# Kernel optimization log

Measured on AMD Instinct MI355X. Metric: run time of the kernel, lower is better.

The kernel has to match this reference:

```python
import jax, jax.numpy as jnp
import numpy as np

N = 100000
E = 1600000
F_IN = 128
HDIM = 64
HEADS = 8
C1 = HDIM // HEADS  # 8 per-head channels in conv1
NUM_CLASSES = 2
NUM_GRAPHS = 64
NEG_SLOPE = 0.2


def setup_inputs() -> dict:
    key = jax.random.key(0)
    ks = jax.random.split(key, 12)
    x = jax.random.normal(ks[0], (N, F_IN), dtype=jnp.float32)
    edge_index = jax.random.randint(ks[1], (2, E), 0, N, dtype=jnp.int64)
    batch = jnp.sort(jax.random.randint(ks[2], (N,), 0, NUM_GRAPHS, dtype=jnp.int64))
    # conv1 params (Glorot-ish scale)
    W1 = jax.random.normal(ks[3], (F_IN, HEADS * C1), dtype=jnp.float32) * (1.0 / np.sqrt(F_IN))
    att_src1 = jax.random.normal(ks[4], (HEADS, C1), dtype=jnp.float32) * 0.1
    att_dst1 = jax.random.normal(ks[5], (HEADS, C1), dtype=jnp.float32) * 0.1
    b1 = jnp.zeros((HEADS * C1,), dtype=jnp.float32)
    # conv2 params (1 head, no concat)
    W2 = jax.random.normal(ks[6], (HDIM, 1 * NUM_CLASSES), dtype=jnp.float32) * (1.0 / np.sqrt(HDIM))
    att_src2 = jax.random.normal(ks[7], (1, NUM_CLASSES), dtype=jnp.float32) * 0.1
    att_dst2 = jax.random.normal(ks[8], (1, NUM_CLASSES), dtype=jnp.float32) * 0.1
    b2 = jnp.zeros((NUM_CLASSES,), dtype=jnp.float32)
    return {"x": x, "edge_index": edge_index, "batch": batch,
            "W1": W1, "att_src1": att_src1, "att_dst1": att_dst1, "b1": b1,
            "W2": W2, "att_src2": att_src2, "att_dst2": att_dst2, "b2": b2}


def gat_conv(x, src, dst, W, a_src, a_dst, b, heads, ch, concat):
    # PyG GATConv: linear proj -> per-edge attention -> segment softmax over dst -> scatter-add
    n = x.shape[0]
    h = (x @ W).reshape(n, heads, ch)                      # [N,H,C]
    alpha_s = jnp.einsum('nhc,hc->nh', h, a_src)           # [N,H]
    alpha_d = jnp.einsum('nhc,hc->nh', h, a_dst)           # [N,H]
    e = jax.nn.leaky_relu(alpha_s[src] + alpha_d[dst], NEG_SLOPE)  # [E,H]
    m = jax.ops.segment_max(e, dst, num_segments=n)        # stable softmax per dst
    e = jnp.exp(e - m[dst])
    denom = jax.ops.segment_sum(e, dst, num_segments=n) + 1e-16
    alpha = e / denom[dst]                                 # [E,H]
    msg = h[src] * alpha[:, :, None]                       # [E,H,C]
    out = jax.ops.segment_sum(msg, dst, num_segments=n)    # [N,H,C]
    if concat:
        out = out.reshape(n, heads * ch)
    else:
        out = out.mean(axis=1)
    return out + b


def reference(x, edge_index, batch, W1, att_src1, att_dst1, b1, W2, att_src2, att_dst2, b2):
    # PyG GATConv default add_self_loops=True
    loops = jnp.arange(N, dtype=edge_index.dtype)
    src = jnp.concatenate([edge_index[0], loops])
    dst = jnp.concatenate([edge_index[1], loops])
    h = gat_conv(x, src, dst, W1, att_src1, att_dst1, b1, HEADS, C1, concat=True)
    h = jax.nn.relu(h)
    # F.dropout with training=False (eval mode) -> identity
    h = gat_conv(h, src, dst, W2, att_src2, att_dst2, b2, 1, NUM_CLASSES, concat=False)
    # global_mean_pool over batch ids
    sums = jax.ops.segment_sum(h, batch, num_segments=NUM_GRAPHS)
    cnts = jax.ops.segment_sum(jnp.ones((N,), h.dtype), batch, num_segments=NUM_GRAPHS)
    pooled = sums / jnp.maximum(cnts, 1.0)[:, None]        # [G, num_classes]
    return jax.nn.log_softmax(pooled, axis=1)
```

## Files before the change

### kernel.cpp

```cpp
#include <hip/hip_runtime.h>
#include <hip/hip_bf16.h>
#include <hip/hip_fp16.h>
#include <math.h>

#define NN 100000
#define EE 1600000
#define ET 1700000
#define NEG_SLOPE 0.2f
#define XS_STRIDE 136
#define L2E 1.44269504088896f

#define BKB 8
#define BKSZ 256
#define NBUCK 391
#define SLAB 8192
#define PAD 32
#define EPT2 16
#define CHUNK2 (256 * EPT2)
#define NCH2 ((ET + CHUNK2 - 1) / CHUNK2)

typedef _Float16 f16;
typedef f16 f16x8 __attribute__((ext_vector_type(8)));
typedef float f32x4 __attribute__((ext_vector_type(4)));
typedef float f32x2 __attribute__((ext_vector_type(2)));

__device__ __forceinline__ float leaky(float v) {
    return v > 0.f ? v : NEG_SLOPE * v;
}
__device__ __forceinline__ unsigned char enc_fp8(float v) {
    int pk = __builtin_amdgcn_cvt_pk_fp8_f32(v, 0.f, 0, false);
    return (unsigned char)(pk & 0xff);
}


__global__ __launch_bounds__(256) void convert_w_kernel(
        const float* __restrict__ W1, f16* __restrict__ wt,
        unsigned char* __restrict__ nrec) {
    int i = blockIdx.x * 256 + threadIdx.x;
    if (i < 128 * 64) {
        int n = i >> 7, k = i & 127;
        wt[n * 128 + k] = (f16)W1[k * 64 + n];
    }
    if (blockIdx.x == 0 && threadIdx.x < 8) {
        uint4* dr = (uint4*)(nrec + (size_t)NN * 128);
        dr[threadIdx.x] = make_uint4(0u, 0u, 0xFC00u, 0u);
    }
}

__global__ __launch_bounds__(256) void gemm1_mfma(
        const float* __restrict__ x, const f16* __restrict__ wt,
        const float* __restrict__ att_s, const float* __restrict__ att_d,
        unsigned char* __restrict__ nrec) {
    __shared__ f16 xs[64 * XS_STRIDE];
    const int tid = threadIdx.x;
    const int node0 = blockIdx.x * 64;
    for (int i = tid; i < 64 * 64; i += 256) {
        int r = i >> 6, cp = i & 63;
        int n = node0 + r;
        float2 v = (n < NN) ? ((const float2*)x)[(long)n * 64 + cp]
                            : make_float2(0.f, 0.f);
        xs[r * XS_STRIDE + 2 * cp]     = (f16)v.x;
        xs[r * XS_STRIDE + 2 * cp + 1] = (f16)v.y;
    }
    __syncthreads();
    const int wv = tid >> 6;
    const int lane = tid & 63;
    const int n16 = lane & 15;
    const int quad = lane >> 4;
    f16x8 bf[4][4];
#pragma unroll
    for (int t = 0; t < 4; ++t)
#pragma unroll
        for (int kk = 0; kk < 4; ++kk)
            bf[t][kk] = *(const f16x8*)(wt + ((t * 16 + n16) * 128 + kk * 32 + quad * 8));
    f32x4 acc[4] = {{0,0,0,0},{0,0,0,0},{0,0,0,0},{0,0,0,0}};
#pragma unroll
    for (int kk = 0; kk < 4; ++kk) {
        f16x8 af = *(const f16x8*)(xs + ((wv * 16 + n16) * XS_STRIDE + kk * 32 + quad * 8));
#pragma unroll
        for (int t = 0; t < 4; ++t)
            acc[t] = __builtin_amdgcn_mfma_f32_16x16x32_f16(af, bf[t][kk], acc[t], 0, 0, 0);
    }
    float ats[4], atd[4];
#pragma unroll
    for (int t = 0; t < 4; ++t) {
        ats[t] = att_s[t * 16 + n16];
        atd[t] = att_d[t * 16 + n16];
    }
    const int head = (n16 >> 3);
    const int chpos = n16 & 7;
#pragma unroll
    for (int t = 0; t < 4; ++t)
#pragma unroll
        for (int r = 0; r < 4; ++r) {
            int m = node0 + wv * 16 + quad * 4 + r;
            bool ok = (m < NN);
            if (ok)
                nrec[(size_t)m * 128 + (t * 2 + head) * 16 + chpos] =
                    enc_fp8(acc[t][r]);
            float vs = acc[t][r] * ats[t];
            float vd = acc[t][r] * atd[t];
            vs += __shfl_xor(vs, 1, 64); vd += __shfl_xor(vd, 1, 64);
            vs += __shfl_xor(vs, 2, 64); vd += __shfl_xor(vd, 2, 64);
            vs += __shfl_xor(vs, 4, 64); vd += __shfl_xor(vd, 4, 64);
            if (ok && chpos == 0) {
                unsigned char* nb = nrec + (size_t)m * 128 + (t * 2 + head) * 16;
                *(__half*)(nb + 8)  = __float2half_rn(vs * L2E);
                *(float*)(nb + 12) = vd * L2E;
            }
        }
}

__global__ __launch_bounds__(256) void bucket_fill(
        const int* __restrict__ ei, int* __restrict__ bcur,
        unsigned* __restrict__ gpay) {
    __shared__ int lcnt[NBUCK];
    __shared__ int gbase[NBUCK];
    const int tid = threadIdx.x;
    for (int i = tid; i < NBUCK; i += 256) lcnt[i] = 0;
    __syncthreads();
    const int base = blockIdx.x * CHUNK2 + tid;
    unsigned pay[EPT2];
    int bk[EPT2], pos[EPT2];
#pragma unroll
    for (int k = 0; k < EPT2; ++k) {
        int e = base + k * 256;
        if (e < ET) {
            int s, d;
            if (e < EE) {
                s = __builtin_nontemporal_load(ei + e);
                d = __builtin_nontemporal_load(ei + EE + e);
            } else { s = d = e - EE; }
            int b = d >> BKB;
            bk[k] = b;
            pay[k] = ((unsigned)(d & (BKSZ - 1)) << 17) | (unsigned)s;
            pos[k] = atomicAdd(&lcnt[b], 1);
        } else bk[k] = -1;
    }
    __syncthreads();
    for (int i = tid; i < NBUCK; i += 256)
        gbase[i] = lcnt[i] ? (i * SLAB + atomicAdd(&bcur[i * PAD], lcnt[i])) : 0;
    __syncthreads();
#pragma unroll
    for (int k = 0; k < EPT2; ++k)
        if (bk[k] >= 0) gpay[gbase[bk[k]] + pos[k]] = pay[k];
}

__global__ __launch_bounds__(256) void fine_csr(
        const unsigned* __restrict__ gpay, const int* __restrict__ bcur,
        int* __restrict__ rowptr, int* __restrict__ rowend,
        int* __restrict__ csr_src) {
    __shared__ int cnt[BKSZ];
    __shared__ int ts[256];
    const int b = blockIdx.x;
    const int tid = threadIdx.x;
    const int off = b * SLAB;
    int blen = bcur[b * PAD];
    if (blen > SLAB) blen = SLAB;
    const int d0 = b << BKB;
    cnt[tid] = 0;
    __syncthreads();
    for (int i = tid; i < blen; i += 256)
        atomicAdd(&cnt[gpay[off + i] >> 17], 1);
    __syncthreads();
    int v = cnt[tid];
    int vp = (v + 7) & ~7;
    ts[tid] = vp;
    __syncthreads();
    for (int o = 1; o < 256; o <<= 1) {
        int u = (tid >= o) ? ts[tid - o] : 0;
        __syncthreads();
        ts[tid] += u;
        __syncthreads();
    }
    int excl = ts[tid] - vp;
    if (excl + vp > SLAB) vp = v;
    cnt[tid] = excl;
    int d = d0 + tid;
    if (d < NN) {
        rowptr[d] = off + excl;
        rowend[d] = off + excl + v;
    }
    for (int i = v; i < vp; ++i) csr_src[off + excl + i] = NN;
    __syncthreads();
    for (int i = tid; i < blen; i += 256) {
        unsigned pay = gpay[off + i];
        int pos = atomicAdd(&cnt[pay >> 17], 1);
        csr_src[off + pos] = (int)(pay & 0x1FFFFu);
    }
}

__global__ __launch_bounds__(256) void conv1_fused_kernel(
        const int* __restrict__ rowptr, const int* __restrict__ rowend,
        const int* __restrict__ csr_src, const unsigned char* __restrict__ nrec,
        const float* __restrict__ b1, const float* __restrict__ W2,
        const float* __restrict__ as2, const float* __restrict__ ad2,
        float4* __restrict__ rec) {
    const int tid = threadIdx.x;
    const int wv = tid >> 6;
    const int c = tid & 63;
    const int slot = c >> 3;
    const int hd = c & 7;
    int n0 = __builtin_amdgcn_readfirstlane((blockIdx.x * 4 + wv) * 2);
    int n1 = n0 + 1;
    const float adA = *(const float*)(nrec + ((size_t)n0 << 7) + (hd << 4) + 12);
    const float adB = *(const float*)(nrec + ((size_t)n1 << 7) + (hd << 4) + 12);
    int jA = rowptr[n0];
    int jB = rowptr[n1];
    int eA = jA + ((rowend[n0] - jA + 7) & ~7);
    int eB = jB + ((rowend[n1] - jB + 7) & ~7);
    float accA[8] = {0.f,0.f,0.f,0.f,0.f,0.f,0.f,0.f};
    float accB[8] = {0.f,0.f,0.f,0.f,0.f,0.f,0.f,0.f};
    float lA = 0.f, lB = 0.f;

#define STEP1(j, ad, l, acc)                                                 \
    {                                                                        \
        int src = csr_src[(j) + slot];                                       \
        uint4 v = *(const uint4*)(nrec + (((size_t)src << 7) | (hd << 4)));  \
        unsigned short ush = (unsigned short)v.z;                            \
        float as = __half2float(*(const __half*)&ush);                       \
        float p = exp2f(leaky(as + (ad)));                                   \
        f32x2 f01 = __builtin_amdgcn_cvt_pk_f32_fp8((int)v.x, 0);            \
        f32x2 f23 = __builtin_amdgcn_cvt_pk_f32_fp8((int)v.x, 1);            \
        f32x2 f45 = __builtin_amdgcn_cvt_pk_f32_fp8((int)v.y, 0);            \
        f32x2 f67 = __builtin_amdgcn_cvt_pk_f32_fp8((int)v.y, 1);            \
        (l) += p;                                                            \
        acc[0] += p * f01.x; acc[1] += p * f01.y;                            \
        acc[2] += p * f23.x; acc[3] += p * f23.y;                            \
        acc[4] += p * f45.x; acc[5] += p * f45.y;                            \
        acc[6] += p * f67.x; acc[7] += p * f67.y;                            \
        (j) += 8;                                                            \
    }

    while (jA < eA && jB < eB) {
        STEP1(jA, adA, lA, accA);
        STEP1(jB, adB, lB, accB);
    }
    while (jA < eA) STEP1(jA, adA, lA, accA);
    while (jB < eB) STEP1(jB, adB, lB, accB);
#undef STEP1

    const int sb0 = slot & 1, sb1 = slot & 2, sb2 = slot & 4;
    float h4A[4], h4B[4];
#pragma unroll
    for (int i = 0; i < 4; ++i) {
        float xa0 = accA[i]     + __shfl_xor(accA[i], 8, 64);
        float xa1 = accA[i + 4] + __shfl_xor(accA[i + 4], 8, 64);
        h4A[i] = sb0 ? xa1 : xa0;
        float xb0 = accB[i]     + __shfl_xor(accB[i], 8, 64);
        float xb1 = accB[i + 4] + __shfl_xor(accB[i + 4], 8, 64);
        h4B[i] = sb0 ? xb1 : xb0;
    }
    float h2A[2], h2B[2];
#pragma unroll
    for (int i = 0; i < 2; ++i) {
        float xa0 = h4A[i]     + __shfl_xor(h4A[i], 16, 64);
        float xa1 = h4A[i + 2] + __shfl_xor(h4A[i + 2], 16, 64);
        h2A[i] = sb1 ? xa1 : xa0;
        float xb0 = h4B[i]     + __shfl_xor(h4B[i], 16, 64);
        float xb1 = h4B[i + 2] + __shfl_xor(h4B[i + 2], 16, 64);
        h2B[i] = sb1 ? xb1 : xb0;
    }
    float ya0 = h2A[0] + __shfl_xor(h2A[0], 32, 64);
    float ya1 = h2A[1] + __shfl_xor(h2A[1], 32, 64);
    float aA = sb2 ? ya1 : ya0;
    float yb0 = h2B[0] + __shfl_xor(h2B[0], 32, 64);
    float yb1 = h2B[1] + __shfl_xor(h2B[1], 32, 64);
    float aB = sb2 ? yb1 : yb0;
    lA += __shfl_xor(lA, 8, 64); lA += __shfl_xor(lA, 16, 64); lA += __shfl_xor(lA, 32, 64);
    lB += __shfl_xor(lB, 8, 64); lB += __shfl_xor(lB, 16, 64); lB += __shfl_xor(lB, 32, 64);
    int ch = (hd << 3) + ((slot & 1) << 2) + (slot & 2) + ((slot >> 2) & 1);
    float invA = 1.f / (lA + 1e-16f);
    float invB = 1.f / (lB + 1e-16f);
    float bb = b1[ch];
    float2 w = ((const float2*)W2)[ch];
    float vA = fmaxf(aA * invA + bb, 0.f);
    float vB = fmaxf(aB * invB + bb, 0.f);
    float rA0 = vA * w.x, rA1 = vA * w.y;
    float rB0 = vB * w.x, rB1 = vB * w.y;
#pragma unroll
    for (int off = 1; off < 64; off <<= 1) {
        rA0 += __shfl_xor(rA0, off, 64);
        rA1 += __shfl_xor(rA1, off, 64);
        rB0 += __shfl_xor(rB0, off, 64);
        rB1 += __shfl_xor(rB1, off, 64);
    }
    if (c == 0) {
        rec[n0] = make_float4((rA0 * as2[0] + rA1 * as2[1]) * L2E, rA0, rA1,
                              (rA0 * ad2[0] + rA1 * ad2[1]) * L2E);
        rec[n1] = make_float4((rB0 * as2[0] + rB1 * as2[1]) * L2E, rB0, rB1,
                              (rB0 * ad2[0] + rB1 * ad2[1]) * L2E);
    }
}

__global__ __launch_bounds__(256) void conv2_pool_kernel(
        const int* __restrict__ rowptr, const int* __restrict__ rowend,
        const int* __restrict__ csr_src, const float4* __restrict__ rec,
        const int* __restrict__ batch,
        float* __restrict__ pooled ) {
    __shared__ float ls[192];
    int tid = threadIdx.x;
    if (tid < 192) ls[tid] = 0.f;
    __syncthreads();
    int n = blockIdx.x * 256 + tid;
    if (n < NN) {
        float adn = rec[n].w;
        int jb = rowptr[n], je = rowend[n];
        float l0 = 0.f, l1 = 0.f, l2 = 0.f, l3 = 0.f;
        float x0 = 0.f, x1 = 0.f, x2 = 0.f, x3 = 0.f;
        float y0 = 0.f, y1 = 0.f, y2 = 0.f, y3 = 0.f;
        int j = jb;
        for (; j + 3 < je; j += 4) {
            float4 ra = rec[csr_src[j]];
            float4 rb = rec[csr_src[j + 1]];
            float4 rc = rec[csr_src[j + 2]];
            float4 rd = rec[csr_src[j + 3]];
            float pa = exp2f(leaky(ra.x + adn));
            float pb = exp2f(leaky(rb.x + adn));
            float pc = exp2f(leaky(rc.x + adn));
            float pd = exp2f(leaky(rd.x + adn));
            l0 += pa; x0 += pa * ra.y; y0 += pa * ra.z;
            l1 += pb; x1 += pb * rb.y; y1 += pb * rb.z;
            l2 += pc; x2 += pc * rc.y; y2 += pc * rc.z;
            l3 += pd; x3 += pd * rd.y; y3 += pd * rd.z;
        }
        for (; j < je; ++j) {
            float4 ra = rec[csr_src[j]];
            float pa = exp2f(leaky(ra.x + adn));
            l0 += pa; x0 += pa * ra.y; y0 += pa * ra.z;
        }
        float l = (l0 + l1) + (l2 + l3);
        float xx = (x0 + x1) + (x2 + x3);
        float yy = (y0 + y1) + (y2 + y3);
        float inv = 1.f / (l + 1e-16f);
        int g = batch[n];
        atomicAdd(&ls[g * 2],     xx * inv);
        atomicAdd(&ls[g * 2 + 1], yy * inv);
        atomicAdd(&ls[128 + g],   1.f);
    }
    __syncthreads();
    if (tid < 192) atomicAdd(&pooled[tid], ls[tid]);
}

__global__ __launch_bounds__(64) void final_kernel(
        const float* __restrict__ pooled, const float* __restrict__ b2,
        float* __restrict__ out) {
    int g = threadIdx.x;
    if (g >= 64) return;
    float c = pooled[128 + g];
    float denom = c > 1.f ? c : 1.f;
    float p0 = pooled[g * 2] / denom + b2[0];
    float p1 = pooled[g * 2 + 1] / denom + b2[1];
    float m = fmaxf(p0, p1);
    float lse = m + logf(expf(p0 - m) + expf(p1 - m));
    out[g * 2] = p0 - lse;
    out[g * 2 + 1] = p1 - lse;
}

extern "C" void kernel_launch(void* const* d_in, const int* in_sizes, int n_in,
                              void* d_out, int out_size, void* d_ws, size_t ws_size,
                              hipStream_t stream) {
    const float* x   = (const float*)d_in[0];
    const int*   ei  = (const int*)d_in[1];
    const int*   bat = (const int*)d_in[2];
    const float* W1  = (const float*)d_in[3];
    const float* as1 = (const float*)d_in[4];
    const float* ad1 = (const float*)d_in[5];
    const float* b1  = (const float*)d_in[6];
    const float* W2  = (const float*)d_in[7];
    const float* as2 = (const float*)d_in[8];
    const float* ad2 = (const float*)d_in[9];
    const float* b2  = (const float*)d_in[10];
    float* out = (float*)d_out;

    float* ws = (float*)d_ws;
    const long off_nrec   = 0;
    const long off_wt     = off_nrec + (long)(NN + 1) * 32;
    const long off_rec    = off_wt + 4096;
    const long off_rowptr = off_rec + (long)NN * 4;
    const long off_rowend = off_rowptr + NN;
    const long off_gpay   = off_rowend + NN;
    const long off_csr    = off_gpay + (long)NBUCK * SLAB;
    const long off_zero   = off_csr + (long)NBUCK * SLAB;
    const long off_bcur   = off_zero;
    const long off_pool   = off_bcur + NBUCK * PAD;
    const long zero_elems = off_pool + 192 - off_zero;

    hipMemsetAsync(ws + off_zero, 0, zero_elems * sizeof(float), stream);

    convert_w_kernel<<<32, 256, 0, stream>>>(W1, (f16*)(ws + off_wt),
                                             (unsigned char*)(ws + off_nrec));
    gemm1_mfma<<<(NN + 63) / 64, 256, 0, stream>>>(
        x, (const f16*)(ws + off_wt), as1, ad1,
        (unsigned char*)(ws + off_nrec));

    bucket_fill<<<NCH2, 256, 0, stream>>>(ei, (int*)(ws + off_bcur),
                                          (unsigned*)(ws + off_gpay));
    fine_csr<<<NBUCK, 256, 0, stream>>>(
        (const unsigned*)(ws + off_gpay), (const int*)(ws + off_bcur),
        (int*)(ws + off_rowptr), (int*)(ws + off_rowend),
        (int*)(ws + off_csr));

    conv1_fused_kernel<<<NN / 8, 256, 0, stream>>>(
        (const int*)(ws + off_rowptr), (const int*)(ws + off_rowend),
        (const int*)(ws + off_csr), (const unsigned char*)(ws + off_nrec),
        b1, W2, as2, ad2, (float4*)(ws + off_rec));

    conv2_pool_kernel<<<(NN + 255) / 256, 256, 0, stream>>>(
        (const int*)(ws + off_rowptr), (const int*)(ws + off_rowend),
        (const int*)(ws + off_csr), (const float4*)(ws + off_rec),
        bat, ws + off_pool);

    final_kernel<<<1, 64, 0, stream>>>(ws + off_pool, b2, out);
}
```

Baseline: 233.9 us.

## Process four nodes per wave in conv1 with butterfly-fold reductions and prefetch conv2 indices

```diff
diff --git a/kernel.cpp b/kernel.cpp
--- a/kernel.cpp
+++ b/kernel.cpp
@@ -25,11 +25,21 @@
 typedef float f32x2 __attribute__((ext_vector_type(2)));
 
 __device__ __forceinline__ float leaky(float v) {
-    return v > 0.f ? v : NEG_SLOPE * v;
+    return fmaxf(v, NEG_SLOPE * v);
 }
 __device__ __forceinline__ unsigned char enc_fp8(float v) {
     int pk = __builtin_amdgcn_cvt_pk_fp8_f32(v, 0.f, 0, false);
     return (unsigned char)(pk & 0xff);
+}
+
+__device__ __forceinline__ void fold8(float (&dst)[8], const float (&X)[8],
+                                      const float (&Y)[8], int sb, int off) {
+#pragma unroll
+    for (int i = 0; i < 8; ++i) {
+        float m = sb ? Y[i] : X[i];
+        float o = sb ? X[i] : Y[i];
+        dst[i] = m + __shfl_xor(o, off, 64);
+    }
 }
 
 
@@ -201,25 +211,29 @@
     const int c = tid & 63;
     const int slot = c >> 3;
     const int hd = c & 7;
-    int n0 = __builtin_amdgcn_readfirstlane((blockIdx.x * 4 + wv) * 2);
-    int n1 = n0 + 1;
-    const float adA = *(const float*)(nrec + ((size_t)n0 << 7) + (hd << 4) + 12);
-    const float adB = *(const float*)(nrec + ((size_t)n1 << 7) + (hd << 4) + 12);
-    int jA = rowptr[n0];
-    int jB = rowptr[n1];
-    int eA = jA + ((rowend[n0] - jA + 7) & ~7);
-    int eB = jB + ((rowend[n1] - jB + 7) & ~7);
-    float accA[8] = {0.f,0.f,0.f,0.f,0.f,0.f,0.f,0.f};
-    float accB[8] = {0.f,0.f,0.f,0.f,0.f,0.f,0.f,0.f};
-    float lA = 0.f, lB = 0.f;
-
-#define STEP1(j, ad, l, acc)                                                 \
+    const int sb0 = slot & 1, sb1 = (slot >> 1) & 1, sb2 = (slot >> 2) & 1;
+    int n0 = __builtin_amdgcn_readfirstlane((blockIdx.x * 4 + wv) * 4);
+    const float adA = *(const float*)(nrec + ((size_t)(n0 + 0) << 7) + (hd << 4) + 12);
+    const float adB = *(const float*)(nrec + ((size_t)(n0 + 1) << 7) + (hd << 4) + 12);
+    const float adC = *(const float*)(nrec + ((size_t)(n0 + 2) << 7) + (hd << 4) + 12);
+    const float adD = *(const float*)(nrec + ((size_t)(n0 + 3) << 7) + (hd << 4) + 12);
+    int jA = rowptr[n0 + 0], eA = jA + ((rowend[n0 + 0] - jA + 7) & ~7);
+    int jB = rowptr[n0 + 1], eB = jB + ((rowend[n0 + 1] - jB + 7) & ~7);
+    int jC = rowptr[n0 + 2], eC = jC + ((rowend[n0 + 2] - jC + 7) & ~7);
+    int jD = rowptr[n0 + 3], eD = jD + ((rowend[n0 + 3] - jD + 7) & ~7);
+    float accA[8] = {0,0,0,0,0,0,0,0}, accB[8] = {0,0,0,0,0,0,0,0};
+    float accC[8] = {0,0,0,0,0,0,0,0}, accD[8] = {0,0,0,0,0,0,0,0};
+    float lA = 0.f, lB = 0.f, lC = 0.f, lD = 0.f;
+
+#define STEP(j, e, ad, l, acc)                                               \
     {                                                                        \
-        int src = csr_src[(j) + slot];                                       \
+        int jj = (j) < (e) - 8 ? (j) : (e) - 8;        \
+        int src = csr_src[jj + slot];                                        \
         uint4 v = *(const uint4*)(nrec + (((size_t)src << 7) | (hd << 4)));  \
         unsigned short ush = (unsigned short)v.z;                            \
         float as = __half2float(*(const __half*)&ush);                       \
         float p = exp2f(leaky(as + (ad)));                                   \
+        p = ((j) < (e)) ? p : 0.f;                                           \
         f32x2 f01 = __builtin_amdgcn_cvt_pk_f32_fp8((int)v.x, 0);            \
         f32x2 f23 = __builtin_amdgcn_cvt_pk_f32_fp8((int)v.x, 1);            \
         f32x2 f45 = __builtin_amdgcn_cvt_pk_f32_fp8((int)v.y, 0);            \
@@ -232,64 +246,53 @@
         (j) += 8;                                                            \
     }
 
-    while (jA < eA && jB < eB) {
-        STEP1(jA, adA, lA, accA);
-        STEP1(jB, adB, lB, accB);
-    }
-    while (jA < eA) STEP1(jA, adA, lA, accA);
-    while (jB < eB) STEP1(jB, adB, lB, accB);
-#undef STEP1
-
-    const int sb0 = slot & 1, sb1 = slot & 2, sb2 = slot & 4;
-    float h4A[4], h4B[4];
+    while (jA < eA || jB < eB || jC < eC || jD < eD) {
+        STEP(jA, eA, adA, lA, accA);
+        STEP(jB, eB, adB, lB, accB);
+        STEP(jC, eC, adC, lC, accC);
+        STEP(jD, eD, adD, lD, accD);
+    }
+#undef STEP
+
+    float P[8], Q[8];
+    fold8(P, accA, accB, sb0, 8);
+    fold8(Q, accC, accD, sb0, 8);
+    float lP, lQ, lm, lo;
+    lm = sb0 ? lB : lA; lo = sb0 ? lA : lB;
+    lP = lm + __shfl_xor(lo, 8, 64);
+    lm = sb0 ? lD : lC; lo = sb0 ? lC : lD;
+    lQ = lm + __shfl_xor(lo, 8, 64);
+    float R[8];
+    fold8(R, P, Q, sb1, 16);
+    lm = sb1 ? lQ : lP; lo = sb1 ? lP : lQ;
+    float l = lm + __shfl_xor(lo, 16, 64);
+    float S[4];
 #pragma unroll
     for (int i = 0; i < 4; ++i) {
-        float xa0 = accA[i]     + __shfl_xor(accA[i], 8, 64);
-        float xa1 = accA[i + 4] + __shfl_xor(accA[i + 4], 8, 64);
-        h4A[i] = sb0 ? xa1 : xa0;
-        float xb0 = accB[i]     + __shfl_xor(accB[i], 8, 64);
-        float xb1 = accB[i + 4] + __shfl_xor(accB[i + 4], 8, 64);
-        h4B[i] = sb0 ? xb1 : xb0;
-    }
-    float h2A[2], h2B[2];
-#pragma unroll
-    for (int i = 0; i < 2; ++i) {
-        float xa0 = h4A[i]     + __shfl_xor(h4A[i], 16, 64);
-        float xa1 = h4A[i + 2] + __shfl_xor(h4A[i + 2], 16, 64);
-        h2A[i] = sb1 ? xa1 : xa0;
-        float xb0 = h4B[i]     + __shfl_xor(h4B[i], 16, 64);
-        float xb1 = h4B[i + 2] + __shfl_xor(h4B[i + 2], 16, 64);
-        h2B[i] = sb1 ? xb1 : xb0;
-    }
-    float ya0 = h2A[0] + __shfl_xor(h2A[0], 32, 64);
-    float ya1 = h2A[1] + __shfl_xor(h2A[1], 32, 64);
-    float aA = sb2 ? ya1 : ya0;
-    float yb0 = h2B[0] + __shfl_xor(h2B[0], 32, 64);
-    float yb1 = h2B[1] + __shfl_xor(h2B[1], 32, 64);
-    float aB = sb2 ? yb1 : yb0;
-    lA += __shfl_xor(lA, 8, 64); lA += __shfl_xor(lA, 16, 64); lA += __shfl_xor(lA, 32, 64);
-    lB += __shfl_xor(lB, 8, 64); lB += __shfl_xor(lB, 16, 64); lB += __shfl_xor(lB, 32, 64);
-    int ch = (hd << 3) + ((slot & 1) << 2) + (slot & 2) + ((slot >> 2) & 1);
-    float invA = 1.f / (lA + 1e-16f);
-    float invB = 1.f / (lB + 1e-16f);
-    float bb = b1[ch];
-    float2 w = ((const float2*)W2)[ch];
-    float vA = fmaxf(aA * invA + bb, 0.f);
-    float vB = fmaxf(aB * invB + bb, 0.f);
-    float rA0 = vA * w.x, rA1 = vA * w.y;
-    float rB0 = vB * w.x, rB1 = vB * w.y;
-#pragma unroll
-    for (int off = 1; off < 64; off <<= 1) {
-        rA0 += __shfl_xor(rA0, off, 64);
-        rA1 += __shfl_xor(rA1, off, 64);
-        rB0 += __shfl_xor(rB0, off, 64);
-        rB1 += __shfl_xor(rB1, off, 64);
-    }
-    if (c == 0) {
-        rec[n0] = make_float4((rA0 * as2[0] + rA1 * as2[1]) * L2E, rA0, rA1,
-                              (rA0 * ad2[0] + rA1 * ad2[1]) * L2E);
-        rec[n1] = make_float4((rB0 * as2[0] + rB1 * as2[1]) * L2E, rB0, rB1,
-                              (rB0 * ad2[0] + rB1 * ad2[1]) * L2E);
+        float m = sb2 ? R[i + 4] : R[i];
+        float o = sb2 ? R[i] : R[i + 4];
+        S[i] = m + __shfl_xor(o, 32, 64);
+    }
+    l += __shfl_xor(l, 32, 64);
+    const int cb = (hd << 3) + sb2 * 4;
+    float inv = 1.f / (l + 1e-16f);
+    float4 bb = *(const float4*)(b1 + cb);
+    float4 w01 = *(const float4*)(W2 + cb * 2);
+    float4 w23 = *(const float4*)(W2 + cb * 2 + 4);
+    float v0 = fmaxf(S[0] * inv + bb.x, 0.f);
+    float v1 = fmaxf(S[1] * inv + bb.y, 0.f);
+    float v2 = fmaxf(S[2] * inv + bb.z, 0.f);
+    float v3 = fmaxf(S[3] * inv + bb.w, 0.f);
+    float r0 = v0 * w01.x + v1 * w01.z + v2 * w23.x + v3 * w23.z;
+    float r1 = v0 * w01.y + v1 * w01.w + v2 * w23.y + v3 * w23.w;
+    r0 += __shfl_xor(r0, 1, 64);  r1 += __shfl_xor(r1, 1, 64);
+    r0 += __shfl_xor(r0, 2, 64);  r1 += __shfl_xor(r1, 2, 64);
+    r0 += __shfl_xor(r0, 4, 64);  r1 += __shfl_xor(r1, 4, 64);
+    r0 += __shfl_xor(r0, 32, 64); r1 += __shfl_xor(r1, 32, 64);
+    if (hd == 0 && sb2 == 0) {
+        int n = n0 + sb1 * 2 + sb0;
+        rec[n] = make_float4((r0 * as2[0] + r1 * as2[1]) * L2E, r0, r1,
+                             (r0 * ad2[0] + r1 * ad2[1]) * L2E);
     }
 }
 
@@ -310,11 +313,16 @@
         float x0 = 0.f, x1 = 0.f, x2 = 0.f, x3 = 0.f;
         float y0 = 0.f, y1 = 0.f, y2 = 0.f, y3 = 0.f;
         int j = jb;
-        for (; j + 3 < je; j += 4) {
-            float4 ra = rec[csr_src[j]];
-            float4 rb = rec[csr_src[j + 1]];
-            float4 rc = rec[csr_src[j + 2]];
-            float4 rd = rec[csr_src[j + 3]];
+        int i0 = csr_src[j], i1 = csr_src[j + 1];
+        int i2 = csr_src[j + 2], i3 = csr_src[j + 3];
+        for (; j + 3 < je; ) {
+            float4 ra = rec[i0];
+            float4 rb = rec[i1];
+            float4 rc = rec[i2];
+            float4 rd = rec[i3];
+            j += 4;
+            i0 = csr_src[j] & 0x1FFFF;     i1 = csr_src[j + 1] & 0x1FFFF;
+            i2 = csr_src[j + 2] & 0x1FFFF; i3 = csr_src[j + 3] & 0x1FFFF;
             float pa = exp2f(leaky(ra.x + adn));
             float pb = exp2f(leaky(rb.x + adn));
             float pc = exp2f(leaky(rc.x + adn));
@@ -401,7 +409,7 @@
         (int*)(ws + off_rowptr), (int*)(ws + off_rowend),
         (int*)(ws + off_csr));
 
-    conv1_fused_kernel<<<NN / 8, 256, 0, stream>>>(
+    conv1_fused_kernel<<<NN / 16, 256, 0, stream>>>(
         (const int*)(ws + off_rowptr), (const int*)(ws + off_rowend),
         (const int*)(ws + off_csr), (const unsigned char*)(ws + off_nrec),
         b1, W2, as2, ad2, (float4*)(ws + off_rec));
```

After: 229.6 us. Within noise of the previous version (-1.8%).
